# Kernel optimization log

Hardware: AMD Instinct MI355X
Metric: run time of the kernel (lower is better)

Reference implementation:

```python
import jax, jax.numpy as jnp
import numpy as np

DIM = 1024
KV_DIM = 768
NUM_HEADS = 16
HEAD_DIM = DIM // NUM_HEADS
EPS = 1e-6


def _rms_norm(h, g):
    var = jnp.mean(h * h, axis=-1, keepdims=True)
    return h * jax.lax.rsqrt(var + EPS) * g


def _rotate_half(t):
    t1, t2 = jnp.split(t, 2, axis=-1)
    return jnp.concatenate((-t2, t1), axis=-1)


def _apply_rope(t, cos, sin):
    # t: [B, L, H, D]; cos/sin: [B, L, D] -> broadcast over heads (unsqueeze_dim=2)
    cos = cos[:, :, None, :]
    sin = sin[:, :, None, :]
    return t * cos + _rotate_half(t) * sin


def setup_inputs() -> dict:
    key = jax.random.key(0)
    ks = jax.random.split(key, 16)
    B, Lq, Lkv = 2, 4096, 1024
    inp = {
        "x": jax.random.normal(ks[0], (B, Lq, DIM), jnp.float32),
        "y": jax.random.normal(ks[1], (B, Lkv, KV_DIM), jnp.float32),
        "x_cos": jax.random.normal(ks[2], (B, Lq, HEAD_DIM), jnp.float32),
        "x_sin": jax.random.normal(ks[3], (B, Lq, HEAD_DIM), jnp.float32),
        "y_cos": jax.random.normal(ks[4], (B, Lkv, HEAD_DIM), jnp.float32),
        "y_sin": jax.random.normal(ks[5], (B, Lkv, HEAD_DIM), jnp.float32),
        # Linear params stored as [in, out] (apply as h @ W + b)
        "Wq": jax.random.normal(ks[6], (DIM, DIM), jnp.float32) * 0.02,
        "bq": jnp.zeros((DIM,), jnp.float32),
        "Wk": jax.random.normal(ks[7], (KV_DIM, DIM), jnp.float32) * 0.02,
        "bk": jnp.zeros((DIM,), jnp.float32),
        "Wv": jax.random.normal(ks[8], (KV_DIM, DIM), jnp.float32) * 0.02,
        "bv": jnp.zeros((DIM,), jnp.float32),
        "Wo": jax.random.normal(ks[9], (DIM, DIM), jnp.float32) * 0.02,
        "bo": jnp.zeros((DIM,), jnp.float32),
        "gq": jnp.ones((DIM,), jnp.float32),   # RMSNorm weight for q
        "gk": jnp.ones((DIM,), jnp.float32),   # RMSNorm weight for k
    }
    return inp


def reference(x, y, x_cos, x_sin, y_cos, y_sin,
              Wq, bq, Wk, bk, Wv, bv, Wo, bo, gq, gk):
    B, Lq, _ = x.shape
    _, Lkv, _ = y.shape
    q = _rms_norm(x @ Wq + bq, gq)              # [B, Lq, DIM]
    k = _rms_norm(y @ Wk + bk, gk)              # [B, Lkv, DIM]
    v = y @ Wv + bv                              # [B, Lkv, DIM]

    q = q.reshape(B, Lq, NUM_HEADS, HEAD_DIM)
    k = k.reshape(B, Lkv, NUM_HEADS, HEAD_DIM)
    v = v.reshape(B, Lkv, NUM_HEADS, HEAD_DIM)

    q = _apply_rope(q, x_cos, x_sin)
    k = _apply_rope(k, y_cos, y_sin)

    scale = HEAD_DIM ** -0.5
    scores = jnp.einsum("blhd,bmhd->bhlm", q, k) * scale   # [B, H, Lq, Lkv]
    probs = jax.nn.softmax(scores, axis=-1)
    out = jnp.einsum("bhlm,bmhd->blhd", probs, v)           # [B, Lq, H, D]
    out = out.reshape(B, Lq, DIM)
    return out @ Wo + bo
```

## Files before the change

### kernel.cpp

```cpp
#include <hip/hip_runtime.h>

typedef __bf16 bf16;
typedef __bf16 bf16x4 __attribute__((ext_vector_type(4)));
typedef __bf16 bf16x8 __attribute__((ext_vector_type(8)));
typedef float  f32x4  __attribute__((ext_vector_type(4)));
typedef float  f32x16 __attribute__((ext_vector_type(16)));
typedef unsigned u32x4 __attribute__((ext_vector_type(4)));

#define NH   16
#define HD   64
#define DQ   1024
#define DKV  768
#define LQ   4096
#define LKV  1024
#define NB   2

__device__ __forceinline__ f32x4 mfma16(bf16x8 a, bf16x8 b, f32x4 c) {
    return __builtin_amdgcn_mfma_f32_16x16x32_bf16(a, b, c, 0, 0, 0);
}
__device__ __forceinline__ f32x16 mfma32(bf16x8 a, bf16x8 b, f32x16 c) {
    return __builtin_amdgcn_mfma_f32_32x32x16_bf16(a, b, c, 0, 0, 0);
}

__device__ __forceinline__ void plswap(unsigned &a, unsigned &b) {
#if __has_builtin(__builtin_amdgcn_permlane32_swap)
    auto r = __builtin_amdgcn_permlane32_swap(a, b, false, false);
    a = (unsigned)r[0]; b = (unsigned)r[1];
#else
    asm volatile("v_permlane32_swap_b32 %0, %1" : "+v"(a), "+v"(b));
#endif
}

#define GLDS16(g, l) __builtin_amdgcn_global_load_lds(                      \
    (const __attribute__((address_space(1))) void*)(g),                     \
    (__attribute__((address_space(3))) void*)(l), 16, 0, 0)

__global__ __launch_bounds__(256) void prep(
        const float* __restrict__ Wq, const float* __restrict__ Wk,
        const float* __restrict__ Wv, const float* __restrict__ Wo,
        bf16* __restrict__ Wq_t, bf16* __restrict__ Wk_t,
        bf16* __restrict__ Wv_t, bf16* __restrict__ Wo_t,
        const float* __restrict__ x, const float* __restrict__ y,
        bf16* __restrict__ xb, bf16* __restrict__ yb,
        int nx8, int ntot8) {
    if (blockIdx.z < 4) {
        __shared__ float tile[32][33];
        const float* in; bf16* out; int K;
        switch (blockIdx.z) {
            case 0:  in = Wq; out = Wq_t; K = DQ;  break;
            case 1:  in = Wk; out = Wk_t; K = DKV; break;
            case 2:  in = Wv; out = Wv_t; K = DKV; break;
            default: in = Wo; out = Wo_t; K = DQ;  break;
        }
        int n0 = blockIdx.x * 32, k0 = blockIdx.y * 32;
        if (k0 >= K) return;
        int tx = threadIdx.x, ty = threadIdx.y;
        for (int yy = 0; yy < 32; yy += 8)
            tile[ty + yy][tx] = in[(size_t)(k0 + ty + yy) * DQ + n0 + tx];
        __syncthreads();
        for (int yy = 0; yy < 32; yy += 8)
            out[(size_t)(n0 + ty + yy) * K + k0 + tx] = (bf16)tile[tx][ty + yy];
    } else {
        int tid = threadIdx.y * 32 + threadIdx.x;
        int flat = (blockIdx.y * 32 + blockIdx.x) * 256 + tid;
        for (int i = flat; i < ntot8; i += 32 * 32 * 256) {
            const float* in; bf16* out; int j;
            if (i < nx8) { in = x; out = xb; j = i; }
            else         { in = y; out = yb; j = i - nx8; }
            float4 a0 = ((const float4*)in)[(size_t)j * 2];
            float4 a1 = ((const float4*)in)[(size_t)j * 2 + 1];
            bf16x8 v = {(bf16)a0.x, (bf16)a0.y, (bf16)a0.z, (bf16)a0.w,
                        (bf16)a1.x, (bf16)a1.y, (bf16)a1.z, (bf16)a1.w};
            ((bf16x8*)out)[j] = v;
        }
    }
}

template <int MODE>
__device__ __forceinline__ void gemm_body(const bf16* __restrict__ A,
                                          const bf16* __restrict__ Bt,
                                          const float* __restrict__ bias,
                                          void* __restrict__ Cv,
                                          int N, int K, int m0) {
    __shared__ bf16 As[128 * 32];
    __shared__ bf16 Bs[128 * 32];
    int tid  = threadIdx.x;
    int lane = tid & 63, w = tid >> 6;
    int quad = lane >> 4, l15 = lane & 15;
    int wm = (w >> 1) * 64, wn = (w & 1) * 64;
    int n0 = blockIdx.x * 128;
    int srow = tid >> 2, scol = (tid & 3) * 8;
    const bf16* Ag = &A [(size_t)(m0 + srow) * K + scol];
    const bf16* Bg = &Bt[(size_t)(n0 + srow) * K + scol];
    bf16* Asw = As + w * 512;
    bf16* Bsw = Bs + w * 512;

    f32x4 acc[4][4] = {};

    for (int k0 = 0; k0 < K; k0 += 32) {
        GLDS16(Ag + k0,                  Asw);
        GLDS16(Ag + (size_t)64 * K + k0, Asw + 2048);
        GLDS16(Bg + k0,                  Bsw);
        GLDS16(Bg + (size_t)64 * K + k0, Bsw + 2048);
        __syncthreads();
        bf16x8 af[4], bfr[4];
#pragma unroll
        for (int i = 0; i < 4; i++)
            af[i] = *(const bf16x8*)&As[(size_t)(wm + i * 16 + l15) * 32 + quad * 8];
#pragma unroll
        for (int j = 0; j < 4; j++)
            bfr[j] = *(const bf16x8*)&Bs[(size_t)(wn + j * 16 + l15) * 32 + quad * 8];
#pragma unroll
        for (int i = 0; i < 4; i++)
#pragma unroll
            for (int j = 0; j < 4; j++)
                acc[i][j] = mfma16(af[i], bfr[j], acc[i][j]);
        __syncthreads();
    }

    bf16*  Cb = (bf16*)Cv;
    float* Cf = (float*)Cv;
#pragma unroll
    for (int i = 0; i < 4; i++)
#pragma unroll
        for (int j = 0; j < 4; j++) {
            int col = n0 + wn + j * 16 + l15;
            float bcol = bias[col];
            if (MODE == 1) {
                int rowb = m0 + wm + i * 16 + quad * 4;
                int bb = rowb >> 10, kv = rowb & 1023;
                int h = col >> 6, d = col & 63;
                bf16x4 val = {(bf16)(acc[i][j][0] + bcol), (bf16)(acc[i][j][1] + bcol),
                              (bf16)(acc[i][j][2] + bcol), (bf16)(acc[i][j][3] + bcol)};
                *(bf16x4*)&Cb[(((size_t)(bb * NH + h) * HD) + d) * LKV + kv] = val;
            } else {
#pragma unroll
                for (int r = 0; r < 4; r++) {
                    int row = m0 + wm + i * 16 + quad * 4 + r;
                    float v = acc[i][j][r] + bcol;
                    if (MODE == 2) Cf[(size_t)row * N + col] = v;
                    else           Cb[(size_t)row * N + col] = (bf16)v;
                }
            }
        }
}

__global__ __launch_bounds__(256) void gemm_qkv(
        const bf16* xb, const bf16* Wq_t, const float* bq, bf16* qbuf,
        const bf16* yb, const bf16* Wk_t, const float* bk, bf16* kbuf,
        const bf16* Wv_t, const float* bv, bf16* vT) {
    int y = blockIdx.y;
    if (y < 64)      gemm_body<0>(xb, Wq_t, bq, qbuf, DQ, DQ,  y * 128);
    else if (y < 80) gemm_body<0>(yb, Wk_t, bk, kbuf, DQ, DKV, (y - 64) * 128);
    else             gemm_body<1>(yb, Wv_t, bv, vT,   DQ, DKV, (y - 80) * 128);
}
__global__ __launch_bounds__(256) void gemm_o(const bf16* A, const bf16* Bt,
                                              const float* bias, void* Cv) {
    gemm_body<2>(A, Bt, bias, Cv, DQ, DQ, blockIdx.y * 128);
}

__global__ __launch_bounds__(256) void rmsnorm_rope3(bf16* __restrict__ qb,
                                                     bf16* __restrict__ kb,
                                                     const float* __restrict__ gq,
                                                     const float* __restrict__ gk,
                                                     const float* __restrict__ xc,
                                                     const float* __restrict__ xs,
                                                     const float* __restrict__ yc,
                                                     const float* __restrict__ ys) {
    int w = threadIdx.x >> 6, lane = threadIdx.x & 63;
    int row = blockIdx.x * 4 + w;
    bf16* t; const float *g, *cs, *sn;
    if (row < NB * LQ) {
        t = qb + (size_t)row * DQ; g = gq;
        cs = xc + (size_t)row * HD; sn = xs + (size_t)row * HD;
    } else {
        int r2 = row - NB * LQ;
        t = kb + (size_t)r2 * DQ; g = gk;
        cs = yc + (size_t)r2 * HD; sn = ys + (size_t)r2 * HD;
    }
    int c0 = lane * 16;
    bf16x8 a0 = *(const bf16x8*)&t[c0];
    bf16x8 a1 = *(const bf16x8*)&t[c0 + 8];
    float vv[16], ss = 0.f;
#pragma unroll
    for (int j = 0; j < 8; j++) { vv[j] = (float)a0[j]; vv[8 + j] = (float)a1[j]; }
#pragma unroll
    for (int j = 0; j < 16; j++) ss += vv[j] * vv[j];
#pragma unroll
    for (int off = 32; off >= 1; off >>= 1) ss += __shfl_xor(ss, off, 64);
    float rms = rsqrtf(ss * (1.0f / 1024.0f) + 1e-6f);
    float nv[16];
#pragma unroll
    for (int j = 0; j < 16; j++) nv[j] = vv[j] * rms * g[c0 + j];
    int d0 = (lane & 3) * 16;
    float sgn = (lane & 2) ? 1.f : -1.f;
    bf16x8 o0, o1;
#pragma unroll
    for (int j = 0; j < 16; j++) {
        float pv = __shfl_xor(nv[j], 2, 64);
        float r = nv[j] * cs[d0 + j] + sgn * pv * sn[d0 + j];
        if (j < 8) o0[j] = (bf16)r; else o1[j - 8] = (bf16)r;
    }
    *(bf16x8*)&t[c0]     = o0;
    *(bf16x8*)&t[c0 + 8] = o1;
}

__global__ __launch_bounds__(256, 4) void attn_kern(const bf16* __restrict__ q,
                                                    const bf16* __restrict__ k,
                                                    const bf16* __restrict__ vT,
                                                    bf16* __restrict__ o) {
    __shared__ bf16 Ks[2][64][64];
    __shared__ bf16 Vs[2][64][64];
    int tid = threadIdx.x, w = tid >> 6, lane = tid & 63;
    int l31 = lane & 31, hi = lane >> 5;
    int b = blockIdx.z, h = blockIdx.y, qt = blockIdx.x;
    int qrow = qt * 128 + w * 32 + l31;
    int sw8 = (l31 & 7) << 3;

    bf16x8 qf[4];
    {
        const bf16* qg = &q[((size_t)(b * LQ) + qrow) * DQ + h * HD + hi * 8];
#pragma unroll
        for (int kc = 0; kc < 4; kc++) {
            bf16x8 tq = *(const bf16x8*)(qg + kc * 16);
#pragma unroll
            for (int e = 0; e < 8; e++) tq[e] = (bf16)((float)tq[e] * 0.125f);
            qf[kc] = tq;
        }
    }

    int rb = w * 16;
    int srow = rb + (lane >> 3);
    int sl = (lane & 7) ^ (srow & 7);
    const bf16* kg0 = &k[((size_t)(b * LKV) + srow) * DQ + h * HD + sl * 8];
    const bf16* vg0 = &vT[(((size_t)(b * NH + h) * HD) + srow) * LKV + sl * 8];

    GLDS16(kg0,                   &Ks[0][rb][0]);
    GLDS16(kg0 + (size_t)8 * DQ,  &Ks[0][rb + 8][0]);
    GLDS16(vg0,                   &Vs[0][rb][0]);
    GLDS16(vg0 + (size_t)8 * LKV, &Vs[0][rb + 8][0]);
    __syncthreads();

    f32x16 O0 = {}, O1 = {};
    float m_run = -1e30f, l_run = 0.f;

    for (int i = 0; i < 16; i++) {
        int cur = i & 1;
        if (i < 15) {
            int nxt = cur ^ 1;
            size_t ko = (size_t)(i + 1) * 64 * DQ;
            int    vo = (i + 1) * 64;
            GLDS16(kg0 + ko,                   &Ks[nxt][rb][0]);
            GLDS16(kg0 + ko + (size_t)8 * DQ,  &Ks[nxt][rb + 8][0]);
            GLDS16(vg0 + vo,                   &Vs[nxt][rb][0]);
            GLDS16(vg0 + vo + (size_t)8 * LKV, &Vs[nxt][rb + 8][0]);
        }
#pragma unroll
        for (int t = 0; t < 2; t++) {
            f32x16 S = {};
            {
                int krow = t * 32 + l31;
                __builtin_amdgcn_s_setprio(1);
#pragma unroll
                for (int kc = 0; kc < 4; kc++) {
                    bf16x8 kf = *(const bf16x8*)&Ks[cur][krow][(kc * 16 + hi * 8) ^ sw8];
                    S = mfma32(kf, qf[kc], S);
                }
                __builtin_amdgcn_s_setprio(0);
            }
            float m01 = fmaxf(fmaxf(S[0], S[1]),  fmaxf(S[2], S[3]));
            float m23 = fmaxf(fmaxf(S[4], S[5]),  fmaxf(S[6], S[7]));
            float m45 = fmaxf(fmaxf(S[8], S[9]),  fmaxf(S[10], S[11]));
            float m67 = fmaxf(fmaxf(S[12], S[13]), fmaxf(S[14], S[15]));
            float pmax = fmaxf(fmaxf(m01, m23), fmaxf(m45, m67));
            pmax = fmaxf(pmax, __shfl_xor(pmax, 32, 64));
            if (!__all(pmax - m_run <= 8.f)) {
                float mn = fmaxf(m_run, pmax);
                float alpha = __expf(m_run - mn);
                m_run = mn; l_run *= alpha;
#pragma unroll
                for (int r = 0; r < 16; r++) { O0[r] *= alpha; O1[r] *= alpha; }
            }
            float rs = 0.f;
#pragma unroll
            for (int r = 0; r < 16; r++) { S[r] = __expf(S[r] - m_run); rs += S[r]; }
            rs += __shfl_xor(rs, 32, 64);
            l_run += rs;
            unsigned dw[8];
#pragma unroll
            for (int g = 0; g < 4; g++)
#pragma unroll
                for (int hh = 0; hh < 2; hh++) {
                    unsigned d_;
                    asm("v_cvt_pk_bf16_f32 %0, %1, %2"
                        : "=v"(d_) : "v"(S[4 * g + 2 * hh]), "v"(S[4 * g + 2 * hh + 1]));
                    dw[g * 2 + hh] = d_;
                }
#pragma unroll
            for (int kcl = 0; kcl < 2; kcl++) {
                int kc = t * 2 + kcl;
                unsigned a0 = dw[(2 * kcl) * 2 + 0], b0 = dw[(2 * kcl + 1) * 2 + 0];
                unsigned a1 = dw[(2 * kcl) * 2 + 1], b1 = dw[(2 * kcl + 1) * 2 + 1];
                plswap(a0, b0);
                plswap(a1, b1);
                u32x4 pw = {a0, a1, b0, b1};
                bf16x8 pb = __builtin_bit_cast(bf16x8, pw);
                int vcol = (kc * 16 + hi * 8) ^ sw8;
                bf16x8 vf0 = *(const bf16x8*)&Vs[cur][l31][vcol];
                bf16x8 vf1 = *(const bf16x8*)&Vs[cur][32 + l31][vcol];
                __builtin_amdgcn_s_setprio(1);
                O0 = mfma32(vf0, pb, O0);
                O1 = mfma32(vf1, pb, O1);
                __builtin_amdgcn_s_setprio(0);
            }
        }
        if (i < 15) __syncthreads();
    }

    float inv = 1.0f / l_run;
    size_t ob = ((size_t)(b * LQ) + qrow) * DQ + h * HD;
#pragma unroll
    for (int td = 0; td < 2; td++) {
        const f32x16& O = td ? O1 : O0;
#pragma unroll
        for (int g = 0; g < 4; g++) {
            bf16x4 ov = {(bf16)(O[4 * g + 0] * inv), (bf16)(O[4 * g + 1] * inv),
                         (bf16)(O[4 * g + 2] * inv), (bf16)(O[4 * g + 3] * inv)};
            *(bf16x4*)&o[ob + td * 32 + g * 8 + hi * 4] = ov;
        }
    }
}

extern "C" void kernel_launch(void* const* d_in, const int* in_sizes, int n_in,
                              void* d_out, int out_size, void* d_ws, size_t ws_size,
                              hipStream_t stream) {
    const float* x     = (const float*)d_in[0];
    const float* y     = (const float*)d_in[1];
    const float* x_cos = (const float*)d_in[2];
    const float* x_sin = (const float*)d_in[3];
    const float* y_cos = (const float*)d_in[4];
    const float* y_sin = (const float*)d_in[5];
    const float* Wq    = (const float*)d_in[6];
    const float* bq    = (const float*)d_in[7];
    const float* Wk    = (const float*)d_in[8];
    const float* bk    = (const float*)d_in[9];
    const float* Wv    = (const float*)d_in[10];
    const float* bv    = (const float*)d_in[11];
    const float* Wo    = (const float*)d_in[12];
    const float* bo    = (const float*)d_in[13];
    const float* gq    = (const float*)d_in[14];
    const float* gk    = (const float*)d_in[15];

    char* ws = (char*)d_ws;
    bf16* Wq_t = (bf16*)ws;  ws += (size_t)DQ * DQ * 2;
    bf16* Wk_t = (bf16*)ws;  ws += (size_t)DQ * DKV * 2;
    bf16* Wv_t = (bf16*)ws;  ws += (size_t)DQ * DKV * 2;
    bf16* Wo_t = (bf16*)ws;  ws += (size_t)DQ * DQ * 2;
    bf16* qbuf = (bf16*)ws;  ws += (size_t)NB * LQ * DQ * 2;
    bf16* kbuf = (bf16*)ws;  ws += (size_t)NB * LKV * DQ * 2;
    bf16* vT   = (bf16*)ws;  ws += (size_t)NB * NH * HD * LKV * 2;
    bf16* aout = (bf16*)ws;  ws += (size_t)NB * LQ * DQ * 2;
    bf16* yb   = (bf16*)ws;  ws += (size_t)NB * LKV * DKV * 2;
    bf16* xb   = aout;

    int nx8 = NB * LQ * DQ / 8, ny8 = NB * LKV * DKV / 8;
    prep<<<dim3(32, 32, 5), dim3(32, 8), 0, stream>>>(
        Wq, Wk, Wv, Wo, Wq_t, Wk_t, Wv_t, Wo_t,
        x, y, xb, yb, nx8, nx8 + ny8);

    gemm_qkv<<<dim3(8, 96), 256, 0, stream>>>(
        xb, Wq_t, bq, qbuf, yb, Wk_t, bk, kbuf, Wv_t, bv, vT);

    rmsnorm_rope3<<<NB * (LQ + LKV) / 4, 256, 0, stream>>>(
        qbuf, kbuf, gq, gk, x_cos, x_sin, y_cos, y_sin);

    attn_kern<<<dim3(LQ / 128, NH, NB), 256, 0, stream>>>(qbuf, kbuf, vT, aout);

    gemm_o<<<dim3(DQ / 128, NB * LQ / 128), 256, 0, stream>>>(aout, Wo_t, bo, d_out);
}
```

Before: 282.9 us.

## Double-buffer GEMM LDS loads, swizzle LDS layout, and remap blocks for XCD locality

```diff
diff --git a/kernel.cpp b/kernel.cpp
--- a/kernel.cpp
+++ b/kernel.cpp
@@ -77,39 +77,53 @@
 }
 
 template <int MODE>
-__device__ __forceinline__ void gemm_body(const bf16* __restrict__ A,
+__device__ __forceinline__ void gemm_body(bf16* __restrict__ sm,
+                                          const bf16* __restrict__ A,
                                           const bf16* __restrict__ Bt,
                                           const float* __restrict__ bias,
                                           void* __restrict__ Cv,
-                                          int N, int K, int m0) {
-    __shared__ bf16 As[128 * 32];
-    __shared__ bf16 Bs[128 * 32];
+                                          int N, int K, int m0, int n0) {
+    bf16* As = sm;
+    bf16* Bs = sm + 2 * 4096;
     int tid  = threadIdx.x;
     int lane = tid & 63, w = tid >> 6;
     int quad = lane >> 4, l15 = lane & 15;
     int wm = (w >> 1) * 64, wn = (w & 1) * 64;
-    int n0 = blockIdx.x * 128;
-    int srow = tid >> 2, scol = (tid & 3) * 8;
+    int srow = tid >> 2;
+    int scol = ((tid & 3) ^ (srow & 3)) * 8;
     const bf16* Ag = &A [(size_t)(m0 + srow) * K + scol];
     const bf16* Bg = &Bt[(size_t)(n0 + srow) * K + scol];
-    bf16* Asw = As + w * 512;
-    bf16* Bsw = Bs + w * 512;
+    int woff = w * 512;
+    int fcol = ((quad ^ (l15 & 3)) * 8);
 
     f32x4 acc[4][4] = {};
-
-    for (int k0 = 0; k0 < K; k0 += 32) {
-        GLDS16(Ag + k0,                  Asw);
-        GLDS16(Ag + (size_t)64 * K + k0, Asw + 2048);
-        GLDS16(Bg + k0,                  Bsw);
-        GLDS16(Bg + (size_t)64 * K + k0, Bsw + 2048);
-        __syncthreads();
+    int nit = K >> 5;
+
+#define STAGE(buf, kk) do {                                              \
+        int k0_ = (kk) << 5;                                             \
+        bf16* a_ = As + (buf) * 4096 + woff;                             \
+        bf16* b_ = Bs + (buf) * 4096 + woff;                             \
+        GLDS16(Ag + k0_,                  a_);                           \
+        GLDS16(Ag + (size_t)64 * K + k0_, a_ + 2048);                    \
+        GLDS16(Bg + k0_,                  b_);                           \
+        GLDS16(Bg + (size_t)64 * K + k0_, b_ + 2048);                    \
+    } while (0)
+
+    STAGE(0, 0);
+    __syncthreads();
+
+    for (int t = 0; t < nit; t++) {
+        int cur = t & 1;
+        if (t + 1 < nit) STAGE(cur ^ 1, t + 1);
+        const bf16* Ac = As + cur * 4096;
+        const bf16* Bc = Bs + cur * 4096;
         bf16x8 af[4], bfr[4];
 #pragma unroll
         for (int i = 0; i < 4; i++)
-            af[i] = *(const bf16x8*)&As[(size_t)(wm + i * 16 + l15) * 32 + quad * 8];
+            af[i] = *(const bf16x8*)&Ac[(wm + i * 16 + l15) * 32 + fcol];
 #pragma unroll
         for (int j = 0; j < 4; j++)
-            bfr[j] = *(const bf16x8*)&Bs[(size_t)(wn + j * 16 + l15) * 32 + quad * 8];
+            bfr[j] = *(const bf16x8*)&Bc[(wn + j * 16 + l15) * 32 + fcol];
 #pragma unroll
         for (int i = 0; i < 4; i++)
 #pragma unroll
@@ -117,6 +131,7 @@
                 acc[i][j] = mfma16(af[i], bfr[j], acc[i][j]);
         __syncthreads();
     }
+#undef STAGE
 
     bf16*  Cb = (bf16*)Cv;
     float* Cf = (float*)Cv;
@@ -145,18 +160,25 @@
         }
 }
 
-__global__ __launch_bounds__(256) void gemm_qkv(
+__global__ __launch_bounds__(256, 3) void gemm_qkv(
         const bf16* xb, const bf16* Wq_t, const float* bq, bf16* qbuf,
         const bf16* yb, const bf16* Wk_t, const float* bk, bf16* kbuf,
         const bf16* Wv_t, const float* bv, bf16* vT) {
-    int y = blockIdx.y;
-    if (y < 64)      gemm_body<0>(xb, Wq_t, bq, qbuf, DQ, DQ,  y * 128);
-    else if (y < 80) gemm_body<0>(yb, Wk_t, bk, kbuf, DQ, DKV, (y - 64) * 128);
-    else             gemm_body<1>(yb, Wv_t, bv, vT,   DQ, DKV, (y - 80) * 128);
-}
-__global__ __launch_bounds__(256) void gemm_o(const bf16* A, const bf16* Bt,
-                                              const float* bias, void* Cv) {
-    gemm_body<2>(A, Bt, bias, Cv, DQ, DQ, blockIdx.y * 128);
+    __shared__ bf16 sm[4 * 4096];
+    int lin  = blockIdx.y * 8 + blockIdx.x;
+    int work = (lin & 7) * 96 + (lin >> 3);
+    int xt = work & 7, yt = work >> 3;
+    if (yt < 64)      gemm_body<0>(sm, xb, Wq_t, bq, qbuf, DQ, DQ,  yt * 128,        xt * 128);
+    else if (yt < 80) gemm_body<0>(sm, yb, Wk_t, bk, kbuf, DQ, DKV, (yt - 64) * 128, xt * 128);
+    else              gemm_body<1>(sm, yb, Wv_t, bv, vT,   DQ, DKV, (yt - 80) * 128, xt * 128);
+}
+__global__ __launch_bounds__(256, 3) void gemm_o(const bf16* A, const bf16* Bt,
+                                                 const float* bias, void* Cv) {
+    __shared__ bf16 sm[4 * 4096];
+    int lin  = blockIdx.y * 8 + blockIdx.x;
+    int work = (lin & 7) * 64 + (lin >> 3);
+    int xt = work & 7, yt = work >> 3;
+    gemm_body<2>(sm, A, Bt, bias, Cv, DQ, DQ, yt * 128, xt * 128);
 }
 
 __global__ __launch_bounds__(256) void rmsnorm_rope3(bf16* __restrict__ qb,
@@ -213,7 +235,9 @@
     __shared__ bf16 Vs[2][64][64];
     int tid = threadIdx.x, w = tid >> 6, lane = tid & 63;
     int l31 = lane & 31, hi = lane >> 5;
-    int b = blockIdx.z, h = blockIdx.y, qt = blockIdx.x;
+    int lin  = blockIdx.x + (blockIdx.y << 5) + (blockIdx.z << 9);
+    int work = (lin & 7) * 128 + (lin >> 3);
+    int qt = work & 31, h = (work >> 5) & 15, b = work >> 9;
     int qrow = qt * 128 + w * 32 + l31;
     int sw8 = (l31 & 7) << 3;
 
```

Result: faster. 248.5 us (-12.2%).
